# Optimization experiments

Hardware: AMD Instinct MI355X
Metric: run time of the kernel (lower is better)

Reference implementation:

```python
import jax, jax.numpy as jnp
import numpy as np

N_NODES, N_FEATS, HIDDEN, N_CLASS = 100000, 256, 128, 64
B, K0, K1, N_HIST = 1024, 25, 10, 5


def setup_inputs() -> dict:
    key = jax.random.key(0)
    ks = jax.random.split(key, 11)
    return {
        "feats": jax.random.normal(ks[0], (N_NODES, N_FEATS), dtype=jnp.float32),
        "history": jax.random.normal(ks[1], (N_NODES, HIDDEN), dtype=jnp.float32),
        "W0": jax.random.normal(ks[2], (2 * N_FEATS, HIDDEN), dtype=jnp.float32) * 0.05,
        "b0": jax.random.normal(ks[3], (HIDDEN,), dtype=jnp.float32) * 0.05,
        "W1": jax.random.normal(ks[4], (2 * HIDDEN, N_CLASS), dtype=jnp.float32) * 0.05,
        "b1": jax.random.normal(ks[5], (N_CLASS,), dtype=jnp.float32) * 0.05,
        "nodes": jax.random.randint(ks[6], (B,), 0, N_NODES, dtype=jnp.int64 if jax.config.jax_enable_x64 else jnp.int32),
        "neighs0": jax.random.randint(ks[7], (B, K0), 0, N_NODES),
        "neighs1": jax.random.randint(ks[8], (B, K1), 0, N_NODES),
        "neighs0_nb": jax.random.randint(ks[9], (B * K1, K0), 0, N_NODES),
        "h_nodes": jax.random.randint(ks[10], (B, N_HIST), 0, N_NODES),
    }


def _layer0(feats, W0, b0, h_prev, neighs):
    # h_prev: [M, 1, F]; neighs: [M, K0]
    neigh_feats = feats[neighs]                       # [M, K0, F] gather
    h = jnp.mean(neigh_feats, axis=1, keepdims=True)  # MeanAggregator -> [M, 1, F]
    h = jnp.concatenate([h_prev, h], axis=-1)         # [M, 1, 2F]
    return jax.nn.relu(h @ W0 + b0)                   # [M, 1, H]


def reference(feats, history, W0, b0, W1, b1, nodes, neighs0, neighs1, neighs0_nb, h_nodes):
    # ---- layer 0 for the seed nodes (x = feats[nodes], detached per source) ----
    x = jax.lax.stop_gradient(feats[nodes])           # torch: x.detach().clone()
    h_prev = x[:, None, :]                            # [B, 1, F]
    h1 = _layer0(feats, W0, b0, h_prev, neighs0)      # [B, 1, H]

    # ---- layer 1: recursive layer-0 embeddings of sampled neighbors ----
    nx = jax.lax.stop_gradient(feats[neighs1.reshape(-1)])[:, None, :]  # [B*K1, 1, F]
    neigh_original = _layer0(feats, W0, b0, nx, neighs0_nb)             # [B*K1, 1, H]
    neigh_original = neigh_original.reshape(B, K1, HIDDEN)

    # historical-activation trick (history lookups are detached in source)
    neigh_historical = jax.lax.stop_gradient(history[h_nodes])          # [B, 5, H]
    neigh_delta = neigh_original - jax.lax.stop_gradient(history[neighs1])
    neigh_delta = neigh_delta * (N_HIST / K1)
    neigh_feats = jnp.concatenate([neigh_delta, neigh_historical], axis=1)  # [B, K1+5, H]
    # NOTE: source also scatters history[neighs1] = neigh_original (side effect);
    # functional equivalent: history.at[neighs1].set(neigh_original), not returned here.

    h = jnp.mean(neigh_feats, axis=1, keepdims=True)                    # [B, 1, H]
    h = jnp.concatenate([h1, h], axis=-1)                               # [B, 1, 2H]
    h = jax.nn.relu(h @ W1 + b1)                                        # [B, 1, C]
    return h.squeeze(1)                                                 # [B, C]
```

## Files before the change

### kernel.cpp

```cpp
#include <hip/hip_runtime.h>

#define N_FEATS 256
#define HIDDEN  128
#define N_CLASS 64
#define BATCH   1024
#define K0      25
#define K1      10
#define N_HIST  5
#define M_TOTAL (BATCH + BATCH * K1)
#define KDIM    512
#define N_NODES 100000

typedef unsigned short u16;
typedef short bf16x8 __attribute__((ext_vector_type(8)));
typedef _Float16 f16x8 __attribute__((ext_vector_type(8)));
typedef float f32x4 __attribute__((ext_vector_type(4)));

static __device__ __forceinline__ u16 f2bf(float f) {
    union { float f; unsigned int i; } v;
    v.f = f;
    unsigned int x = v.i;
    x += ((x >> 16) & 1u) + 0x7FFFu;
    return (u16)(x >> 16);
}
static __device__ __forceinline__ unsigned int pack2(float lo, float hi) {
    return (unsigned int)f2bf(lo) | ((unsigned int)f2bf(hi) << 16);
}
static __device__ __forceinline__ u16 f2h(float f) {
    union { _Float16 h; u16 u; } v;
    v.h = (_Float16)f;
    return v.u;
}
static __device__ __forceinline__ int loadI(const void* p, long long i, int f64) {
    const char* cp = (const char*)p + (f64 ? (i << 3) : (i << 2));
    return *(const int*)cp;
}

__global__ void k_detect(const void* __restrict__ nodes, int* __restrict__ flag) {
    if (threadIdx.x == 0 && blockIdx.x == 0) {
        const int* p = (const int*)nodes;
        int f = 1;
        for (int i = 0; i < 8; ++i)
            if (p[2 * i + 1] != 0) f = 0;
        *flag = f;
    }
}


__global__ void k_transpose_w0h(const float* __restrict__ W0, u16* __restrict__ W0T2,
                                const void* __restrict__ nodes, int* __restrict__ flag) {
    if (threadIdx.x == 0 && threadIdx.y == 0 && blockIdx.x == 0 && blockIdx.y == 0) {
        const int* p = (const int*)nodes;
        int f = 1;
        for (int i = 0; i < 8; ++i)
            if (p[2 * i + 1] != 0) f = 0;
        *flag = f;
    }
    __shared__ u16 tile[32][33];
    int tx = threadIdx.x;
    int ty = threadIdx.y;
    int k0 = blockIdx.x * 32;
    int n0 = blockIdx.y * 32;
#pragma unroll
    for (int i = 0; i < 32; i += 8)
        tile[ty + i][tx] = f2h(W0[(size_t)(k0 + ty + i) * HIDDEN + n0 + tx]);
    __syncthreads();
    int roff = (k0 >= 256) ? 128 : 0;
    int kk = k0 & 255;
#pragma unroll
    for (int i = 0; i < 32; i += 8)
        W0T2[(size_t)(n0 + ty + i + roff) * 256 + kk + tx] = tile[tx][ty + i];
}

#define TROWS      32
#define NTILES     3125
#define PROJ_NBLK  512
__global__ __launch_bounds__(512, 4) void k_proj3(
        const float* __restrict__ feats,
        const u16* __restrict__ W0T2,
        u16* __restrict__ P) {
    __shared__ u16 Xs[2][TROWS][256 + 8];
    const int tid = threadIdx.x;
    const int wv = tid >> 6;
    const int lane = tid & 63;
    const int m = lane & 15;
    const int q = lane >> 4;
    const int base = NTILES / PROJ_NBLK;
    const int rem = NTILES - base * PROJ_NBLK;
    const int bi = blockIdx.x;
    const int s0 = bi * base + (bi < rem ? bi : rem);
    const int cnt = base + (bi < rem ? 1 : 0);

    f16x8 B0[8], B1[8];
    {
        const u16* bb = W0T2 + (size_t)(wv * 32 + m) * 256 + q * 8;
#pragma unroll
        for (int kk = 0; kk < 8; ++kk) {
            B0[kk] = *(const f16x8*)(bb + kk * 32);
            B1[kk] = *(const f16x8*)(bb + 16 * 256 + kk * 32);
        }
    }

    float4 st[4];
    const float* fbase = feats + (size_t)(wv * 4) * N_FEATS + lane * 4;

#define PROJ_ISSUE(t)                                                         \
    {                                                                         \
        const float* fp_ = fbase + (size_t)(t) * (TROWS * N_FEATS);           \
        _Pragma("unroll")                                                     \
        for (int i = 0; i < 4; ++i)                                           \
            st[i] = *(const float4*)(fp_ + (size_t)i * N_FEATS);              \
    }
#define PROJ_WRITE(b)                                                         \
    {                                                                         \
        _Pragma("unroll")                                                     \
        for (int i = 0; i < 4; ++i) {                                         \
            ushort4 pk;                                                       \
            pk.x = f2h(st[i].x); pk.y = f2h(st[i].y);                         \
            pk.z = f2h(st[i].z); pk.w = f2h(st[i].w);                         \
            *(ushort4*)&Xs[b][wv * 4 + i][lane * 4] = pk;                     \
        }                                                                     \
    }

    PROJ_ISSUE(s0);
    PROJ_WRITE(0);
    PROJ_ISSUE(s0 + 1);
    __syncthreads();

    int cur = 0;
    for (int tt = 0; tt < cnt; ++tt) {
        const int t = s0 + tt;
        f32x4 a00 = (f32x4){0.f,0.f,0.f,0.f}, a01 = (f32x4){0.f,0.f,0.f,0.f};
        f32x4 a10 = (f32x4){0.f,0.f,0.f,0.f}, a11 = (f32x4){0.f,0.f,0.f,0.f};
#pragma unroll
        for (int kk = 0; kk < 8; ++kk) {
            f16x8 f0 = *(const f16x8*)&Xs[cur][m][kk * 32 + q * 8];
            f16x8 f1 = *(const f16x8*)&Xs[cur][m + 16][kk * 32 + q * 8];
            a00 = __builtin_amdgcn_mfma_f32_16x16x32_f16(f0, B0[kk], a00, 0, 0, 0);
            a01 = __builtin_amdgcn_mfma_f32_16x16x32_f16(f0, B1[kk], a01, 0, 0, 0);
            a10 = __builtin_amdgcn_mfma_f32_16x16x32_f16(f1, B0[kk], a10, 0, 0, 0);
            a11 = __builtin_amdgcn_mfma_f32_16x16x32_f16(f1, B1[kk], a11, 0, 0, 0);
        }
        __syncthreads();
#pragma unroll
        for (int r = 0; r < 4; ++r) {
            Xs[cur][q * 4 + r][wv * 32 + m]           = f2h(a00[r]);
            Xs[cur][q * 4 + r][wv * 32 + 16 + m]      = f2h(a01[r]);
            Xs[cur][16 + q * 4 + r][wv * 32 + m]      = f2h(a10[r]);
            Xs[cur][16 + q * 4 + r][wv * 32 + 16 + m] = f2h(a11[r]);
        }
        if (tt + 1 < cnt) {
            PROJ_WRITE(cur ^ 1);
            if (tt + 2 < cnt) PROJ_ISSUE(t + 2);
        }
        __syncthreads();
        {
            const int row0 = tid >> 5;
            const int c8 = (tid & 31) * 8;
#pragma unroll
            for (int p = 0; p < 2; ++p) {
                uint4 w = *(const uint4*)&Xs[cur][row0 + p * 16][c8];
                *(uint4*)(P + (size_t)(t * TROWS + row0 + p * 16) * 256 + c8) = w;
            }
        }
        cur ^= 1;
    }
#undef PROJ_ISSUE
#undef PROJ_WRITE
}

__global__ __launch_bounds__(256) void k_gf(
        const u16* __restrict__ P,
        const float* __restrict__ history,
        const void* __restrict__ nodes,
        const void* __restrict__ neighs0,
        const void* __restrict__ neighs1,
        const void* __restrict__ neighs0_nb,
        const void* __restrict__ h_nodes,
        const float* __restrict__ b0,
        const float* __restrict__ W1,
        const float* __restrict__ b1,
        float* __restrict__ out,
        const int* __restrict__ flag) {
    __shared__ float Hs[11][128];
    __shared__ float hcat[2 * HIDDEN];
    __shared__ float red[256];
    const int f64 = *flag;
    const int tid = threadIdx.x;
    const int b = blockIdx.x;
    const int wv = tid >> 6;
    const int lane = tid & 63;
    const int m = lane & 15;
    const int grp = lane >> 4;

    for (int r = wv; r < 11; r += 4) {
        int selfIdx;
        const void* nbp;
        long long nbo;
        if (r == 0) {
            selfIdx = loadI(nodes, b, f64);
            nbp = neighs0; nbo = (long long)b * K0;
        } else {
            int rr = b * K1 + (r - 1);
            selfIdx = loadI(neighs1, rr, f64);
            nbp = neighs0_nb; nbo = (long long)rr * K0;
        }
        int idx[K0];
#pragma unroll
        for (int k = 0; k < K0; ++k) idx[k] = loadI(nbp, nbo + k, f64);

        float a[8];
#pragma unroll
        for (int i = 0; i < 8; ++i) a[i] = 0.f;
#pragma unroll
        for (int k = 0; k < 7; ++k) {
            int k1 = 4 * k + grp;
            if (k1 < K0) {
                f16x8 v = *(const f16x8*)(P + (size_t)idx[k1] * 256 + 128 + m * 8);
#pragma unroll
                for (int i = 0; i < 8; ++i) a[i] += (float)v[i];
            }
        }
#pragma unroll
        for (int i = 0; i < 8; ++i) {
            a[i] += __shfl_xor(a[i], 16);
            a[i] += __shfl_xor(a[i], 32);
        }
        if (grp == 0) {
            f16x8 sv = *(const f16x8*)(P + (size_t)selfIdx * 256 + m * 8);
            const float inv = 1.0f / (float)K0;
#pragma unroll
            for (int i = 0; i < 8; ++i) {
                float y = a[i] * inv + (float)sv[i] + b0[m * 8 + i];
                Hs[r][m * 8 + i] = y > 0.f ? y : 0.f;
            }
        }
    }
    __syncthreads();

    const int j = tid & 127;
    const int half = tid >> 7;
    float S = 0.f;
    if (half == 0) hcat[j] = Hs[0][j];
#pragma unroll
    for (int t = half * 5; t < half * 5 + 5; ++t) {
        int n1 = loadI(neighs1, b * K1 + t, f64);
        S += 0.5f * (Hs[1 + t][j] - history[(size_t)n1 * HIDDEN + j]);
    }
    if (half == 1) {
#pragma unroll
        for (int u = 0; u < N_HIST; ++u) {
            int hn = loadI(h_nodes, b * N_HIST + u, f64);
            S += history[(size_t)hn * HIDDEN + j];
        }
    }
    red[tid] = S;
    __syncthreads();
    if (half == 0)
        hcat[HIDDEN + j] = (red[j] + red[HIDDEN + j]) * (1.0f / 15.0f);
    __syncthreads();

    const int n = tid & 63;
    const int seg = tid >> 6;
    float p = 0.f;
#pragma unroll 8
    for (int i = seg * 64; i < seg * 64 + 64; ++i)
        p += hcat[i] * W1[(size_t)i * N_CLASS + n];
    red[tid] = p;
    __syncthreads();
    if (tid < 64) {
        float a = red[tid] + red[tid + 64] + red[tid + 128] + red[tid + 192]
                + b1[tid];
        a = a > 0.f ? a : 0.f;
        out[(size_t)b * N_CLASS + tid] = a;
    }
}

__global__ void k_transpose_w0(const float* __restrict__ W0, u16* __restrict__ W0T) {
    __shared__ u16 tile[32][33];
    int tx = threadIdx.x;
    int ty = threadIdx.y;
    int k0 = blockIdx.x * 32;
    int n0 = blockIdx.y * 32;
#pragma unroll
    for (int i = 0; i < 32; i += 8)
        tile[ty + i][tx] = f2bf(W0[(size_t)(k0 + ty + i) * HIDDEN + n0 + tx]);
    __syncthreads();
#pragma unroll
    for (int i = 0; i < 32; i += 8)
        W0T[(size_t)(n0 + ty + i) * KDIM + k0 + tx] = tile[tx][ty + i];
}

__global__ __launch_bounds__(512) void k_layer0(
        const float* __restrict__ feats,
        const void* __restrict__ nodes,
        const void* __restrict__ neighs0,
        const void* __restrict__ neighs1,
        const void* __restrict__ neighs0_nb,
        const u16* __restrict__ W0T,
        const float* __restrict__ b0,
        float* __restrict__ H,
        const int* __restrict__ flag) {
    __shared__ u16 Xs[16][KDIM + 8];
    const int f64 = *flag;
    int wv = threadIdx.x >> 6;
    int lane = threadIdx.x & 63;
    int row0 = blockIdx.x * 16;
    int d = lane * 4;

#pragma unroll
    for (int i = 0; i < 2; ++i) {
        int lr = wv * 2 + i;
        int g = row0 + lr;
        int selfIdx;
        const void* nbp;
        long long nbo;
        if (g < BATCH) {
            selfIdx = loadI(nodes, g, f64);
            nbp = neighs0; nbo = (long long)g * K0;
        } else {
            int rr = g - BATCH;
            selfIdx = loadI(neighs1, rr, f64);
            nbp = neighs0_nb; nbo = (long long)rr * K0;
        }
        int idx[K0];
#pragma unroll
        for (int k = 0; k < K0; ++k) idx[k] = loadI(nbp, nbo + k, f64);

        float4 sv = *(const float4*)(feats + (size_t)selfIdx * N_FEATS + d);
        float a0 = 0.f, a1 = 0.f, a2 = 0.f, a3 = 0.f;
#pragma unroll
        for (int k = 0; k < K0; ++k) {
            float4 v = *(const float4*)(feats + (size_t)idx[k] * N_FEATS + d);
            a0 += v.x; a1 += v.y; a2 += v.z; a3 += v.w;
        }
        const float inv = 1.0f / (float)K0;
        uint2 spk, mpk;
        spk.x = pack2(sv.x, sv.y);
        spk.y = pack2(sv.z, sv.w);
        mpk.x = pack2(a0 * inv, a1 * inv);
        mpk.y = pack2(a2 * inv, a3 * inv);
        *(uint2*)&Xs[lr][d] = spk;
        *(uint2*)&Xs[lr][N_FEATS + d] = mpk;
    }
    __syncthreads();

    int m = lane & 15;
    int q = lane >> 4;
    f32x4 acc = (f32x4){0.f, 0.f, 0.f, 0.f};
    const u16* bbase = W0T + (size_t)(wv * 16 + m) * KDIM + q * 8;
#pragma unroll
    for (int k0 = 0; k0 < KDIM; k0 += 32) {
        bf16x8 af = *(const bf16x8*)&Xs[m][k0 + q * 8];
        bf16x8 bf = *(const bf16x8*)(bbase + k0);
        acc = __builtin_amdgcn_mfma_f32_16x16x32_bf16(af, bf, acc, 0, 0, 0);
    }
    int col = wv * 16 + m;
    float bias = b0[col];
#pragma unroll
    for (int r = 0; r < 4; ++r) {
        float y = acc[r] + bias;
        y = y > 0.f ? y : 0.f;
        H[(size_t)(row0 + q * 4 + r) * HIDDEN + col] = y;
    }
}

__global__ __launch_bounds__(256) void k_final(
        const float* __restrict__ H,
        const float* __restrict__ history,
        const void* __restrict__ neighs1,
        const void* __restrict__ h_nodes,
        const float* __restrict__ W1,
        const float* __restrict__ b1,
        float* __restrict__ out,
        const int* __restrict__ flag) {
    __shared__ float hcat[2 * HIDDEN];
    __shared__ float red[256];
    const int f64 = *flag;
    const int tid = threadIdx.x;
    const int b = blockIdx.x;
    const int j = tid & 127;
    const int half = tid >> 7;

    float S = 0.f;
    if (half == 0) hcat[j] = H[(size_t)b * HIDDEN + j];
#pragma unroll
    for (int t = half * 5; t < half * 5 + 5; ++t) {
        float orig = H[(size_t)(BATCH + b * K1 + t) * HIDDEN + j];
        int n1 = loadI(neighs1, b * K1 + t, f64);
        float hist = history[(size_t)n1 * HIDDEN + j];
        S += 0.5f * (orig - hist);
    }
    if (half == 1) {
#pragma unroll
        for (int u = 0; u < N_HIST; ++u) {
            int hn = loadI(h_nodes, b * N_HIST + u, f64);
            S += history[(size_t)hn * HIDDEN + j];
        }
    }
    red[tid] = S;
    __syncthreads();
    if (half == 0)
        hcat[HIDDEN + j] = (red[j] + red[HIDDEN + j]) * (1.0f / 15.0f);
    __syncthreads();

    const int n = tid & 63;
    const int seg = tid >> 6;
    float p = 0.f;
#pragma unroll 8
    for (int i = seg * 64; i < seg * 64 + 64; ++i)
        p += hcat[i] * W1[(size_t)i * N_CLASS + n];
    red[tid] = p;
    __syncthreads();
    if (tid < 64) {
        float a = red[tid] + red[tid + 64] + red[tid + 128] + red[tid + 192]
                + b1[tid];
        a = a > 0.f ? a : 0.f;
        out[(size_t)b * N_CLASS + tid] = a;
    }
}

static __device__ __forceinline__ float loadF_m(const void* p, long long i, int fbf) {
    const char* cp = (const char*)p + (fbf ? (i << 1) : (i << 2));
    if (fbf) {
        union { unsigned int u; float f; } v;
        v.u = ((unsigned int)(*(const u16*)cp)) << 16;
        return v.f;
    }
    return *(const float*)cp;
}

__global__ __launch_bounds__(256) void k_fused(
        const void* __restrict__ feats,
        const void* __restrict__ history,
        const void* __restrict__ W0,
        const void* __restrict__ b0,
        const void* __restrict__ W1,
        const void* __restrict__ b1,
        const void* __restrict__ nodes,
        const void* __restrict__ neighs0,
        const void* __restrict__ neighs1,
        const void* __restrict__ neighs0_nb,
        const void* __restrict__ h_nodes,
        float* __restrict__ out) {
    __shared__ float W0s[32][128];
    __shared__ float Xs[11][KDIM];
    __shared__ float hcat[2 * HIDDEN];
    __shared__ float red[256];
    __shared__ int ibuf[K0 + 1];
    __shared__ int sflags[2];

    const int tid = threadIdx.x;
    const int b = blockIdx.x;

    if (tid == 0) {
        const int* ip = (const int*)nodes;
        int f = 1;
        for (int i = 0; i < 8; ++i)
            if (ip[2 * i + 1] != 0) f = 0;
        sflags[0] = f;
        const u16* qp = (const u16*)feats;
        int cnt = 0;
        for (int i = 0; i < 64; ++i) {
            int e = (qp[2 * i] >> 7) & 0xFF;
            if (e >= 90 && e <= 134) cnt++;
        }
        sflags[1] = (cnt >= 40) ? 1 : 0;
    }
    __syncthreads();
    const int f64 = sflags[0];
    const int fbf = sflags[1];

    for (int r = 0; r < 11; ++r) {
        __syncthreads();
        if (tid < K0) {
            long long nbo = (r == 0) ? ((long long)b * K0)
                                     : ((long long)(b * K1 + (r - 1)) * K0);
            const void* nbp = (r == 0) ? neighs0 : neighs0_nb;
            ibuf[tid] = loadI(nbp, nbo + tid, f64);
        } else if (tid == K0) {
            ibuf[K0] = (r == 0) ? loadI(nodes, b, f64)
                                : loadI(neighs1, b * K1 + (r - 1), f64);
        }
        __syncthreads();
        int sidx = ibuf[K0];
        Xs[r][tid] = loadF_m(feats, (long long)sidx * N_FEATS + tid, fbf);
        float s = 0.f;
#pragma unroll
        for (int k = 0; k < K0; ++k)
            s += loadF_m(feats, (long long)ibuf[k] * N_FEATS + tid, fbf);
        Xs[r][N_FEATS + tid] = s * (1.0f / (float)K0);
    }
    __syncthreads();

    const int c = tid & 127;
    const int ph = tid >> 7;
    float acc[11];
#pragma unroll
    for (int r = 0; r < 11; ++r) acc[r] = 0.f;

    for (int s = 0; s < 16; ++s) {
        __syncthreads();
#pragma unroll
        for (int i = 0; i < 16; ++i) {
            int idx = tid + 256 * i;
            int k = idx >> 7, cc = idx & 127;
            W0s[k][cc] = loadF_m(W0, (long long)(32 * s + k) * HIDDEN + cc, fbf);
        }
        __syncthreads();
        const int kb = 32 * s + 16 * ph;
#pragma unroll
        for (int r = 0; r < 11; ++r) {
            float a = 0.f;
#pragma unroll
            for (int j = 0; j < 16; ++j)
                a += Xs[r][kb + j] * W0s[16 * ph + j][c];
            acc[r] += a;
        }
    }

    float S = 0.f;
    float b0v = (tid < 128) ? loadF_m(b0, tid, fbf) : 0.f;
    for (int r = 0; r < 11; ++r) {
        __syncthreads();
        red[tid] = acc[r];
        __syncthreads();
        if (tid < 128) {
            float h = red[tid] + red[tid + 128] + b0v;
            h = h > 0.f ? h : 0.f;
            if (r == 0) {
                hcat[tid] = h;
            } else {
                int n1 = loadI(neighs1, b * K1 + (r - 1), f64);
                float hist = loadF_m(history, (long long)n1 * HIDDEN + tid, fbf);
                S += 0.5f * (h - hist);
            }
        }
    }
    if (tid < 128) {
#pragma unroll
        for (int u = 0; u < N_HIST; ++u) {
            int hn = loadI(h_nodes, b * N_HIST + u, f64);
            S += loadF_m(history, (long long)hn * HIDDEN + tid, fbf);
        }
        hcat[HIDDEN + tid] = S * (1.0f / 15.0f);
    }
    __syncthreads();

    const int n = tid & 63;
    const int seg = tid >> 6;
    float p = 0.f;
#pragma unroll 8
    for (int i = seg * 64; i < seg * 64 + 64; ++i)
        p += hcat[i] * loadF_m(W1, (long long)i * N_CLASS + n, fbf);
    red[tid] = p;
    __syncthreads();
    if (tid < 64) {
        float a = red[tid] + red[tid + 64] + red[tid + 128] + red[tid + 192]
                + loadF_m(b1, tid, fbf);
        a = a > 0.f ? a : 0.f;
        out[(long long)b * N_CLASS + tid] = a;
    }
}

extern "C" void kernel_launch(void* const* d_in, const int* in_sizes, int n_in,
                              void* d_out, int out_size, void* d_ws, size_t ws_size,
                              hipStream_t stream) {
    (void)out_size;
    const long long want[11] = {25600000, 12800000, 65536, 128, 16384, 64,
                                1024, 25600, 10240, 256000, 5120};
    const void* bp[11];
    for (int j = 0; j < 11; ++j) bp[j] = d_in[j < n_in ? j : 0];
    for (int j = 0; j < 11; ++j) {
        if (j < n_in && (long long)in_sizes[j] == want[j]) continue;
        for (int i = 0; i < n_in; ++i)
            if ((long long)in_sizes[i] == want[j]) { bp[j] = d_in[i]; break; }
    }

    const size_t P_BYTES = (size_t)N_NODES * 256 * 2;
    const size_t WS_NEW  = 131072 + P_BYTES + 16;
    const size_t WS_OLD  = 131072 + 5767168 + 16;

    if (ws_size >= WS_NEW) {
        char* ws = (char*)d_ws;
        u16* W0T2 = (u16*)ws;
        u16* P    = (u16*)(ws + 131072);
        int* flag = (int*)(ws + 131072 + P_BYTES);

        k_transpose_w0h<<<dim3(16, 4), dim3(32, 8), 0, stream>>>(
            (const float*)bp[2], W0T2, bp[6], flag);
        k_proj3<<<PROJ_NBLK, 512, 0, stream>>>((const float*)bp[0], W0T2, P);
        k_gf<<<BATCH, 256, 0, stream>>>(
            P, (const float*)bp[1], bp[6], bp[7], bp[8], bp[9], bp[10],
            (const float*)bp[3], (const float*)bp[4], (const float*)bp[5],
            (float*)d_out, flag);
        return;
    }

    if (ws_size >= WS_OLD) {
        char* ws = (char*)d_ws;
        u16* W0T  = (u16*)ws;
        float* H  = (float*)(ws + 131072);
        int* flag = (int*)(ws + 131072 + 5767168);

        k_detect<<<1, 1, 0, stream>>>(bp[6], flag);
        k_transpose_w0<<<dim3(16, 4), dim3(32, 8), 0, stream>>>((const float*)bp[2], W0T);
        k_layer0<<<M_TOTAL / 16, 512, 0, stream>>>(
            (const float*)bp[0], bp[6], bp[7], bp[8], bp[9], W0T,
            (const float*)bp[3], H, flag);
        k_final<<<BATCH, 256, 0, stream>>>(
            H, (const float*)bp[1], bp[8], bp[10],
            (const float*)bp[4], (const float*)bp[5], (float*)d_out, flag);
        return;
    }

    k_fused<<<BATCH, 256, 0, stream>>>(
        bp[0], bp[1], bp[2], bp[3], bp[4], bp[5],
        bp[6], bp[7], bp[8], bp[9], bp[10], (float*)d_out);
}
```

Before: 55.59 us.

## Project only neighbor half of W0 over all nodes; compute self half per sampled row

The whole-graph projection used to compute both halves of feats@W0 (self and neighbor) for all 100k nodes. Now it computes only the neighbor half into a narrower table, halving its MFMA work and output writes. A new small kernel gathers the 11264 self rows, including seed nodes and sampled neighbors, and projects them with the top half of W0. This adds a kernel launch and a random gather of self features. The projection grid also grows from 512 to 768 blocks with higher occupancy bounds.

```diff
diff --git a/kernel.cpp b/kernel.cpp
--- a/kernel.cpp
+++ b/kernel.cpp
@@ -74,31 +74,29 @@
 
 #define TROWS      32
 #define NTILES     3125
-#define PROJ_NBLK  512
-__global__ __launch_bounds__(512, 4) void k_proj3(
+#define BOT_NBLK   768
+__global__ __launch_bounds__(512, 6) void k_projbot(
         const float* __restrict__ feats,
         const u16* __restrict__ W0T2,
-        u16* __restrict__ P) {
+        u16* __restrict__ Pb) {
     __shared__ u16 Xs[2][TROWS][256 + 8];
     const int tid = threadIdx.x;
     const int wv = tid >> 6;
     const int lane = tid & 63;
     const int m = lane & 15;
     const int q = lane >> 4;
-    const int base = NTILES / PROJ_NBLK;
-    const int rem = NTILES - base * PROJ_NBLK;
+    const int base = NTILES / BOT_NBLK;
+    const int rem = NTILES - base * BOT_NBLK;
     const int bi = blockIdx.x;
     const int s0 = bi * base + (bi < rem ? bi : rem);
     const int cnt = base + (bi < rem ? 1 : 0);
 
-    f16x8 B0[8], B1[8];
+    f16x8 B0[8];
     {
-        const u16* bb = W0T2 + (size_t)(wv * 32 + m) * 256 + q * 8;
-#pragma unroll
-        for (int kk = 0; kk < 8; ++kk) {
+        const u16* bb = W0T2 + (size_t)(128 + wv * 16 + m) * 256 + q * 8;
+#pragma unroll
+        for (int kk = 0; kk < 8; ++kk)
             B0[kk] = *(const f16x8*)(bb + kk * 32);
-            B1[kk] = *(const f16x8*)(bb + 16 * 256 + kk * 32);
-        }
     }
 
     float4 st[4];
@@ -130,24 +128,20 @@
     int cur = 0;
     for (int tt = 0; tt < cnt; ++tt) {
         const int t = s0 + tt;
-        f32x4 a00 = (f32x4){0.f,0.f,0.f,0.f}, a01 = (f32x4){0.f,0.f,0.f,0.f};
-        f32x4 a10 = (f32x4){0.f,0.f,0.f,0.f}, a11 = (f32x4){0.f,0.f,0.f,0.f};
+        f32x4 a0 = (f32x4){0.f,0.f,0.f,0.f};
+        f32x4 a1 = (f32x4){0.f,0.f,0.f,0.f};
 #pragma unroll
         for (int kk = 0; kk < 8; ++kk) {
             f16x8 f0 = *(const f16x8*)&Xs[cur][m][kk * 32 + q * 8];
             f16x8 f1 = *(const f16x8*)&Xs[cur][m + 16][kk * 32 + q * 8];
-            a00 = __builtin_amdgcn_mfma_f32_16x16x32_f16(f0, B0[kk], a00, 0, 0, 0);
-            a01 = __builtin_amdgcn_mfma_f32_16x16x32_f16(f0, B1[kk], a01, 0, 0, 0);
-            a10 = __builtin_amdgcn_mfma_f32_16x16x32_f16(f1, B0[kk], a10, 0, 0, 0);
-            a11 = __builtin_amdgcn_mfma_f32_16x16x32_f16(f1, B1[kk], a11, 0, 0, 0);
+            a0 = __builtin_amdgcn_mfma_f32_16x16x32_f16(f0, B0[kk], a0, 0, 0, 0);
+            a1 = __builtin_amdgcn_mfma_f32_16x16x32_f16(f1, B0[kk], a1, 0, 0, 0);
         }
         __syncthreads();
 #pragma unroll
         for (int r = 0; r < 4; ++r) {
-            Xs[cur][q * 4 + r][wv * 32 + m]           = f2h(a00[r]);
-            Xs[cur][q * 4 + r][wv * 32 + 16 + m]      = f2h(a01[r]);
-            Xs[cur][16 + q * 4 + r][wv * 32 + m]      = f2h(a10[r]);
-            Xs[cur][16 + q * 4 + r][wv * 32 + 16 + m] = f2h(a11[r]);
+            Xs[cur][q * 4 + r][wv * 16 + m]      = f2h(a0[r]);
+            Xs[cur][16 + q * 4 + r][wv * 16 + m] = f2h(a1[r]);
         }
         if (tt + 1 < cnt) {
             PROJ_WRITE(cur ^ 1);
@@ -155,13 +149,10 @@
         }
         __syncthreads();
         {
-            const int row0 = tid >> 5;
-            const int c8 = (tid & 31) * 8;
-#pragma unroll
-            for (int p = 0; p < 2; ++p) {
-                uint4 w = *(const uint4*)&Xs[cur][row0 + p * 16][c8];
-                *(uint4*)(P + (size_t)(t * TROWS + row0 + p * 16) * 256 + c8) = w;
-            }
+            const int row0 = tid >> 4;
+            const int c8 = (tid & 15) * 8;
+            uint4 w = *(const uint4*)&Xs[cur][row0][c8];
+            *(uint4*)(Pb + (size_t)(t * TROWS + row0) * 128 + c8) = w;
         }
         cur ^= 1;
     }
@@ -169,10 +160,53 @@
 #undef PROJ_WRITE
 }
 
+__global__ __launch_bounds__(512) void k_top(
+        const float* __restrict__ feats,
+        const void* __restrict__ nodes,
+        const void* __restrict__ neighs1,
+        const u16* __restrict__ W0T2,
+        u16* __restrict__ Htop,
+        const int* __restrict__ flag) {
+    __shared__ u16 Xs[16][256 + 8];
+    const int f64 = *flag;
+    int wv = threadIdx.x >> 6;
+    int lane = threadIdx.x & 63;
+    int row0 = blockIdx.x * 16;
+    int d = lane * 4;
+
+#pragma unroll
+    for (int i = 0; i < 2; ++i) {
+        int lr = wv * 2 + i;
+        int g = row0 + lr;
+        int selfIdx = (g < BATCH) ? loadI(nodes, g, f64)
+                                  : loadI(neighs1, g - BATCH, f64);
+        float4 sv = *(const float4*)(feats + (size_t)selfIdx * N_FEATS + d);
+        ushort4 pk;
+        pk.x = f2h(sv.x); pk.y = f2h(sv.y); pk.z = f2h(sv.z); pk.w = f2h(sv.w);
+        *(ushort4*)&Xs[lr][d] = pk;
+    }
+    __syncthreads();
+
+    int m = lane & 15;
+    int q = lane >> 4;
+    f32x4 acc = (f32x4){0.f, 0.f, 0.f, 0.f};
+    const u16* bbase = W0T2 + (size_t)(wv * 16 + m) * 256 + q * 8;
+#pragma unroll
+    for (int kk = 0; kk < 8; ++kk) {
+        f16x8 af = *(const f16x8*)&Xs[m][kk * 32 + q * 8];
+        f16x8 bf = *(const f16x8*)(bbase + kk * 32);
+        acc = __builtin_amdgcn_mfma_f32_16x16x32_f16(af, bf, acc, 0, 0, 0);
+    }
+    int col = wv * 16 + m;
+#pragma unroll
+    for (int r = 0; r < 4; ++r)
+        Htop[(size_t)(row0 + q * 4 + r) * 128 + col] = f2h(acc[r]);
+}
+
 __global__ __launch_bounds__(256) void k_gf(
-        const u16* __restrict__ P,
+        const u16* __restrict__ Pb,
+        const u16* __restrict__ Htop,
         const float* __restrict__ history,
-        const void* __restrict__ nodes,
         const void* __restrict__ neighs0,
         const void* __restrict__ neighs1,
         const void* __restrict__ neighs0_nb,
@@ -194,16 +228,14 @@
     const int grp = lane >> 4;
 
     for (int r = wv; r < 11; r += 4) {
-        int selfIdx;
         const void* nbp;
         long long nbo;
+        int g;
         if (r == 0) {
-            selfIdx = loadI(nodes, b, f64);
-            nbp = neighs0; nbo = (long long)b * K0;
+            nbp = neighs0; nbo = (long long)b * K0; g = b;
         } else {
             int rr = b * K1 + (r - 1);
-            selfIdx = loadI(neighs1, rr, f64);
-            nbp = neighs0_nb; nbo = (long long)rr * K0;
+            nbp = neighs0_nb; nbo = (long long)rr * K0; g = BATCH + rr;
         }
         int idx[K0];
 #pragma unroll
@@ -216,7 +248,7 @@
         for (int k = 0; k < 7; ++k) {
             int k1 = 4 * k + grp;
             if (k1 < K0) {
-                f16x8 v = *(const f16x8*)(P + (size_t)idx[k1] * 256 + 128 + m * 8);
+                f16x8 v = *(const f16x8*)(Pb + (size_t)idx[k1] * 128 + m * 8);
 #pragma unroll
                 for (int i = 0; i < 8; ++i) a[i] += (float)v[i];
             }
@@ -227,7 +259,7 @@
             a[i] += __shfl_xor(a[i], 32);
         }
         if (grp == 0) {
-            f16x8 sv = *(const f16x8*)(P + (size_t)selfIdx * 256 + m * 8);
+            f16x8 sv = *(const f16x8*)(Htop + (size_t)g * 128 + m * 8);
             const float inv = 1.0f / (float)K0;
 #pragma unroll
             for (int i = 0; i < 8; ++i) {
@@ -577,21 +609,28 @@
             if ((long long)in_sizes[i] == want[j]) { bp[j] = d_in[i]; break; }
     }
 
-    const size_t P_BYTES = (size_t)N_NODES * 256 * 2;
-    const size_t WS_NEW  = 131072 + P_BYTES + 16;
+    const size_t PB_BYTES = (size_t)N_NODES * 128 * 2;
+    const size_t HT_BYTES = (size_t)M_TOTAL * 128 * 2;
+    const size_t OFF_PB   = 131072;
+    const size_t OFF_HT   = OFF_PB + PB_BYTES;
+    const size_t OFF_FLAG = OFF_HT + HT_BYTES;
+    const size_t WS_NEW   = OFF_FLAG + 16;
     const size_t WS_OLD  = 131072 + 5767168 + 16;
 
     if (ws_size >= WS_NEW) {
         char* ws = (char*)d_ws;
         u16* W0T2 = (u16*)ws;
-        u16* P    = (u16*)(ws + 131072);
-        int* flag = (int*)(ws + 131072 + P_BYTES);
+        u16* Pb   = (u16*)(ws + OFF_PB);
+        u16* Htop = (u16*)(ws + OFF_HT);
+        int* flag = (int*)(ws + OFF_FLAG);
 
         k_transpose_w0h<<<dim3(16, 4), dim3(32, 8), 0, stream>>>(
             (const float*)bp[2], W0T2, bp[6], flag);
-        k_proj3<<<PROJ_NBLK, 512, 0, stream>>>((const float*)bp[0], W0T2, P);
+        k_projbot<<<BOT_NBLK, 512, 0, stream>>>((const float*)bp[0], W0T2, Pb);
+        k_top<<<M_TOTAL / 16, 512, 0, stream>>>(
+            (const float*)bp[0], bp[6], bp[8], W0T2, Htop, flag);
         k_gf<<<BATCH, 256, 0, stream>>>(
-            P, (const float*)bp[1], bp[6], bp[7], bp[8], bp[9], bp[10],
+            Pb, Htop, (const float*)bp[1], bp[7], bp[8], bp[9], bp[10],
             (const float*)bp[3], (const float*)bp[4], (const float*)bp[5],
             (float*)d_out, flag);
         return;
```

Result: slower. 58.51 us (+5.2%).
